# Performance work log

Measured on AMD Instinct MI355X. Metric: run time of the kernel, lower is better.

## Reference

```python
import jax, jax.numpy as jnp
from jax import lax
import numpy as np

K_IN, K_OUT, H, ML = 32, 16, 256, 80
L_PRE, L_FWD, B = 60, 80, 1024


def gru_cell(x, h, Wih, Whh, bih, bhh):
    # torch GRU gate order: r, z, n
    gi = x @ Wih.T + bih
    gh = h @ Whh.T + bhh
    ir, iz, inn = jnp.split(gi, 3, axis=-1)
    hr, hz, hn = jnp.split(gh, 3, axis=-1)
    r = jax.nn.sigmoid(ir + hr)
    z = jax.nn.sigmoid(iz + hz)
    n = jnp.tanh(inn + r * hn)
    return (1.0 - z) * n + z * h


def setup_inputs() -> dict:
    key = jax.random.key(0)
    ks = jax.random.split(key, 24)
    s = 0.05
    rn = lambda k, shp: (jax.random.normal(k, shp) * s).astype(jnp.float32)
    inp = {
        "pre_x": jax.random.normal(ks[0], (L_PRE, B, K_IN), dtype=jnp.float32),
        "pre_y": jax.random.normal(ks[1], (L_PRE, B, K_OUT), dtype=jnp.float32),
        "forward_x": jax.random.normal(ks[2], (L_FWD, B, K_IN), dtype=jnp.float32),
        # encoder: embedding Linear(k_in+k_out -> H), GRU(H,H)
        "enc_emb_W": rn(ks[3], (H, K_IN + K_OUT)),
        "enc_emb_b": rn(ks[4], (H,)),
        "enc_Wih": rn(ks[5], (3 * H, H)),
        "enc_Whh": rn(ks[6], (3 * H, H)),
        "enc_bih": rn(ks[7], (3 * H,)),
        "enc_bhh": rn(ks[8], (3 * H,)),
        # decoder: embedding Linear(k_out+k_in -> H), attn Linear(2H -> ML),
        # attn_combine Linear(2H -> H), GRU(H,H), out Linear(H -> k_out)
        "dec_emb_W": rn(ks[9], (H, K_OUT + K_IN)),
        "dec_emb_b": rn(ks[10], (H,)),
        "attn_W": rn(ks[11], (ML, 2 * H)),
        "attn_b": rn(ks[12], (ML,)),
        "comb_W": rn(ks[13], (H, 2 * H)),
        "comb_b": rn(ks[14], (H,)),
        "dec_Wih": rn(ks[15], (3 * H, H)),
        "dec_Whh": rn(ks[16], (3 * H, H)),
        "dec_bih": rn(ks[17], (3 * H,)),
        "dec_bhh": rn(ks[18], (3 * H,)),
        "out_W": rn(ks[19], (K_OUT, H)),
        "out_b": rn(ks[20], (K_OUT,)),
    }
    return inp


def reference(pre_x, pre_y, forward_x,
              enc_emb_W, enc_emb_b, enc_Wih, enc_Whh, enc_bih, enc_bhh,
              dec_emb_W, dec_emb_b, attn_W, attn_b, comb_W, comb_b,
              dec_Wih, dec_Whh, dec_bih, dec_bhh, out_W, out_b):
    L_pre, batch, _ = pre_x.shape
    hdim = enc_emb_b.shape[0]
    max_len = attn_b.shape[0]

    # ---- encoder ----
    emb = jnp.concatenate([pre_x, pre_y], axis=2) @ enc_emb_W.T + enc_emb_b  # [L_pre,B,H]
    h0 = jnp.zeros((batch, hdim), dtype=pre_x.dtype)

    def enc_step(h, x):
        h2 = gru_cell(x, h, enc_Wih, enc_Whh, enc_bih, enc_bhh)
        return h2, h2

    enc_h, enc_outs = lax.scan(enc_step, h0, emb)
    # pad encoder outputs to max_length along time (zeros beyond L_pre)
    enc_outputs = jnp.zeros((max_len, batch, hdim), dtype=pre_x.dtype).at[:L_pre].set(enc_outs)
    enc_bmh = enc_outputs.transpose(1, 0, 2)  # [B, ML, H]

    # ---- decoder (dropout inactive: eval mode) ----
    def dec_step(carry, fx):
        y, h = carry
        di = jnp.concatenate([y, fx], axis=-1)            # [B, k_out+k_in]
        e = di @ dec_emb_W.T + dec_emb_b                   # [B, H]
        logits = jnp.concatenate([e, h], axis=-1) @ attn_W.T + attn_b  # [B, ML]
        aw = jax.nn.softmax(logits, axis=-1)
        ctx = jnp.einsum('bm,bmh->bh', aw, enc_bmh)        # [B, H]
        g = jnp.tanh(jnp.concatenate([e, ctx], axis=-1) @ comb_W.T + comb_b)
        h2 = gru_cell(g, h, dec_Wih, dec_Whh, dec_bih, dec_bhh)
        y2 = h2 @ out_W.T + out_b                          # [B, k_out]
        return (y2, h2), y2

    y_init = jnp.zeros_like(pre_y[0])
    _, ys = lax.scan(dec_step, (y_init, enc_h), forward_x)
    return ys  # [L_fwd, B, k_out]
```

## Files before the change

kernel.cpp:

```cpp
#include <hip/hip_runtime.h>
#include <hip/hip_bf16.h>

#define BATCH 1024
#define HD 256
#define MLEN 80
#define LPRE 60
#define LFWD 80
#define KIN 32
#define KOUT 16

typedef unsigned short bf16_t;
typedef __attribute__((ext_vector_type(8))) short bf16x8;
typedef __attribute__((ext_vector_type(4))) float f32x4;
typedef __attribute__((ext_vector_type(4))) unsigned u32x4;

#define MFMA __builtin_amdgcn_mfma_f32_16x16x32_bf16

__device__ __forceinline__ float bf2f(bf16_t v){ return __uint_as_float(((unsigned)v)<<16); }
__device__ __forceinline__ bf16_t f2bf(float f){
    unsigned u = __float_as_uint(f);
    return (bf16_t)((u + 0x7FFFu + ((u>>16)&1u)) >> 16);
}
__device__ __forceinline__ unsigned pack2(float lo, float hi){
    return (unsigned)f2bf(lo) | ((unsigned)f2bf(hi)<<16);
}
__device__ __forceinline__ float bflo(unsigned d){ return __uint_as_float(d<<16); }
__device__ __forceinline__ float bfhi(unsigned d){ return __uint_as_float(d & 0xffff0000u); }
__device__ __forceinline__ float sigm(float x){ return 1.0f/(1.0f+__expf(-x)); }

#define OFF_Z  262144
#define OFF_IN 524288
#define OFF_HN 655360

__global__ void pack_gru(const float* __restrict__ Wih, const float* __restrict__ Whh,
                         bf16_t* __restrict__ dst)
{
    int T = blockIdx.x*256 + threadIdx.x;
    int grp, local;
    if (T < 16384){ grp=0; local=T; }
    else if (T < 32768){ grp=1; local=T-16384; }
    else if (T < 40960){ grp=2; local=T-32768; }
    else { grp=3; local=T-40960; }
    int nkt = (grp<2)?16:8;
    int nt  = local / (nkt*64);
    int rem = local - nt*(nkt*64);
    int kt  = rem >> 6;
    int l   = rem & 63;
    int n   = nt*16 + (l&15);
    int k0  = kt*32 + ((l>>4)<<3);
    unsigned w[4];
    #pragma unroll
    for (int h2=0; h2<4; h2++){
        float v[2];
        #pragma unroll
        for (int s=0; s<2; s++){
            int k = k0 + h2*2 + s;
            if (grp==0)      v[s] = (k<256)? Wih[(size_t)n*HD + k]       : Whh[(size_t)n*HD + (k-256)];
            else if (grp==1) v[s] = (k<256)? Wih[(size_t)(256+n)*HD + k] : Whh[(size_t)(256+n)*HD + (k-256)];
            else if (grp==2) v[s] = Wih[(size_t)(512+n)*HD + k];
            else             v[s] = Whh[(size_t)(512+n)*HD + k];
        }
        w[h2] = pack2(v[0], v[1]);
    }
    uint4 u = {w[0],w[1],w[2],w[3]};
    *(uint4*)((char*)dst + (size_t)T*16) = u;
}

__global__ void pack_B512(const float* __restrict__ W, bf16_t* __restrict__ dst)
{
    int T = blockIdx.x*256 + threadIdx.x;
    int nt = T >> 10, kt = (T>>6)&15, l = T&63;
    int n = nt*16 + (l&15);
    int k0 = kt*32 + ((l>>4)<<3);
    unsigned w[4];
    #pragma unroll
    for (int h2=0; h2<4; h2++)
        w[h2] = pack2(W[(size_t)n*512 + k0+h2*2], W[(size_t)n*512 + k0+h2*2+1]);
    uint4 u = {w[0],w[1],w[2],w[3]};
    *(uint4*)((char*)dst + (size_t)T*16) = u;
}

__global__ void wfuse_kernel(const float* __restrict__ dembW, const float* __restrict__ dembB,
                             const float* __restrict__ outW, const float* __restrict__ outB,
                             float* __restrict__ Wfuse, float* __restrict__ ebias)
{
    int T = blockIdx.x*256 + threadIdx.x;
    if (T < 65536){
        int k = T >> 8, n = T & 255;
        float acc = 0.f;
        #pragma unroll
        for (int o=0;o<16;o++) acc += dembW[(size_t)n*48 + o]*outW[(size_t)o*HD + k];
        Wfuse[(size_t)k*HD + n] = acc;
    } else if (T < 65792){
        int n = T - 65536;
        float acc = dembB[n];
        #pragma unroll
        for (int o=0;o<16;o++) acc += outB[o]*dembW[(size_t)n*48 + o];
        ebias[n] = acc;
    }
}

__global__ void pack_logits(const float* __restrict__ Wfuse, const float* __restrict__ dembW,
                            const float* __restrict__ attW, const float* __restrict__ attB,
                            const float* __restrict__ dembB, const float* __restrict__ ebias,
                            bf16_t* __restrict__ BL, bf16_t* __restrict__ BL0,
                            float* __restrict__ lb, float* __restrict__ lb0)
{
    int T = blockIdx.x*256 + threadIdx.x;
    if (T < 5760){
        int variant = (T < 2880) ? 0 : 1;
        int local = variant ? (T-2880) : T;
        int nt = local/576, rem = local - nt*576;
        int kt = rem >> 6, l = rem & 63;
        int m  = nt*16 + (l&15);
        int k0 = kt*32 + ((l>>4)<<3);
        unsigned w[4];
        #pragma unroll
        for (int h2=0; h2<4; h2++){
            float v[2];
            for (int s=0;s<2;s++){
                int k = k0 + h2*2 + s;
                float acc;
                if (kt < 8){
                    if (variant == 0){
                        acc = attW[(size_t)m*512 + 256 + k];
                        for (int n=0;n<256;n++) acc += Wfuse[(size_t)k*HD + n]*attW[(size_t)m*512 + n];
                    } else {
                        acc = attW[(size_t)m*512 + 256 + k];
                    }
                } else {
                    int kp = k - 256;
                    acc = 0.f;
                    for (int n=0;n<256;n++) acc += dembW[(size_t)n*48 + 16 + kp]*attW[(size_t)m*512 + n];
                }
                v[s] = acc;
            }
            w[h2] = pack2(v[0], v[1]);
        }
        uint4 u = {w[0],w[1],w[2],w[3]};
        bf16_t* d = variant ? BL0 : BL;
        *(uint4*)((char*)d + (size_t)local*16) = u;
    } else if (T < 5840){
        int m = T - 5760;
        float acc = attB[m];
        for (int n=0;n<256;n++) acc += ebias[n]*attW[(size_t)m*512 + n];
        lb[m] = acc;
    } else if (T < 5920){
        int m = T - 5840;
        float acc = attB[m];
        for (int n=0;n<256;n++) acc += dembB[n]*attW[(size_t)m*512 + n];
        lb0[m] = acc;
    }
}

__global__ void pack_gfold(const float* __restrict__ Wfuse, const float* __restrict__ dembW,
                           const float* __restrict__ combW, const float* __restrict__ combB,
                           const float* __restrict__ ebias, const float* __restrict__ dembB,
                           bf16_t* __restrict__ dst, float* __restrict__ cbf, float* __restrict__ cbf0)
{
    int T = blockIdx.x*256 + threadIdx.x;
    if (T < 9216){
        int nt = T/576, rem = T - nt*576;
        int kt = rem >> 6, l = rem & 63;
        int n = nt*16 + (l&15);
        int k0 = kt*32 + ((l>>4)<<3);
        unsigned w[4];
        for (int h2=0; h2<4; h2++){
            float v[2];
            for (int s=0;s<2;s++){
                int k = k0 + h2*2 + s;
                float acc = 0.f;
                if (k < 256){
                    for (int j=0;j<256;j++) acc += Wfuse[(size_t)k*HD + j]*combW[(size_t)n*512 + j];
                } else {
                    int kp = k - 256;
                    for (int j=0;j<256;j++) acc += dembW[(size_t)j*48 + 16 + kp]*combW[(size_t)n*512 + j];
                }
                v[s] = acc;
            }
            w[h2] = pack2(v[0], v[1]);
        }
        uint4 u = {w[0],w[1],w[2],w[3]};
        *(uint4*)((char*)dst + (size_t)T*16) = u;
    } else if (T < 9472){
        int n = T - 9216;
        float acc = combB[n];
        for (int j=0;j<256;j++) acc += ebias[j]*combW[(size_t)n*512 + j];
        cbf[n] = acc;
    } else if (T < 9728){
        int n = T - 9472;
        float acc = combB[n];
        for (int j=0;j<256;j++) acc += dembB[j]*combW[(size_t)n*512 + j];
        cbf0[n] = acc;
    }
}

__global__ void pack_out(const float* __restrict__ outW, bf16_t* __restrict__ dst)
{
    int T = blockIdx.x*256 + threadIdx.x;
    int kt = T >> 6, l = T & 63;
    int n  = l & 15;
    int k0 = kt*32 + ((l>>4)<<3);
    unsigned w[4];
    #pragma unroll
    for (int h2=0; h2<4; h2++)
        w[h2] = pack2(outW[(size_t)n*HD + k0+h2*2], outW[(size_t)n*HD + k0+h2*2+1]);
    uint4 u = {w[0],w[1],w[2],w[3]};
    *(uint4*)((char*)dst + (size_t)T*16) = u;
}

__global__ __launch_bounds__(256) void emb_kernel(
    const float* __restrict__ px, const float* __restrict__ py,
    const float* __restrict__ embW, const float* __restrict__ embB,
    bf16_t* __restrict__ emb)
{
    __shared__ float Ws[256*49];
    __shared__ float xy[16][48];
    __shared__ float bs[256];
    int t = blockIdx.y, b0 = blockIdx.x*16, tid = threadIdx.x;
    for (int i = tid; i < 256*48; i += 256){ int n=i/48, k=i-n*48; Ws[n*49+k]=embW[i]; }
    bs[tid] = embB[tid];
    for (int i = tid; i < 16*48; i += 256){
        int r=i/48, k=i-r*48;
        xy[r][k] = (k<KIN)? px[((size_t)t*BATCH + b0+r)*KIN + k]
                          : py[((size_t)t*BATCH + b0+r)*KOUT + (k-KIN)];
    }
    __syncthreads();
    int n = tid;
    const float* w = &Ws[n*49];
    for (int r=0;r<16;r++){
        float acc = bs[n];
        #pragma unroll
        for (int k=0;k<48;k++) acc += xy[r][k]*w[k];
        emb[((size_t)t*BATCH + b0+r)*HD + n] = f2bf(acc);
    }
}

__global__ void fxconv(const float* __restrict__ fx, bf16_t* __restrict__ dst)
{
    size_t i = (size_t)blockIdx.x*256 + threadIdx.x;
    const float4* s = (const float4*)(fx + i*8);
    float4 a = s[0], b = s[1];
    uint4 u = { pack2(a.x,a.y), pack2(a.z,a.w), pack2(b.x,b.y), pack2(b.z,b.w) };
    *(uint4*)(dst + i*8) = u;
}

__global__ __launch_bounds__(256) void pgemm(
    const bf16_t* __restrict__ enc, const bf16_t* __restrict__ Bcmb,
    bf16_t* __restrict__ P)
{
    __shared__ __align__(16) bf16_t As[16][264];
    __shared__ __align__(16) bf16_t Gs[16][264];
    int tid = threadIdx.x, b0 = blockIdx.x*16, t = blockIdx.y;
    const bf16_t* src = enc + ((size_t)t*BATCH + b0)*HD;
    for (int i = tid; i < 512; i += 256){
        int r = i>>5, c = i&31;
        *(uint4*)&As[r][c*8] = *(const uint4*)(src + (size_t)r*HD + c*8);
    }
    __syncthreads();
    int lane = tid&63, wave = tid>>6;
    const bf16_t* arow = &As[lane&15][(lane>>4)*8];
    size_t loff = (size_t)lane*16;
    #pragma unroll
    for (int u=0; u<4; u++){
        int nt = wave*4 + u;
        f32x4 c = {0,0,0,0};
        #pragma unroll
        for (int k8=0; k8<8; k8++){
            bf16x8 a = *(const bf16x8*)(arow + k8*32);
            bf16x8 b = *(const bf16x8*)((const char*)Bcmb + (size_t)(((nt<<4)+8+k8)<<10) + loff);
            c = MFMA(a, b, c, 0,0,0);
        }
        int n = (nt<<4) + (lane&15);
        #pragma unroll
        for (int q=0;q<4;q++) Gs[((lane>>4)<<2)+q][n] = f2bf(c[q]);
    }
    __syncthreads();
    bf16_t* dst = P + ((size_t)t*BATCH + b0)*HD;
    for (int i = tid; i < 512; i += 256){
        int r = i>>5, c = i&31;
        *(uint4*)(dst + (size_t)r*HD + c*8) = *(const uint4*)&Gs[r][c*8];
    }
}

__global__ __launch_bounds__(512) void gru_step2(
    const bf16_t* __restrict__ A0, const bf16_t* __restrict__ A1,
    const bf16_t* __restrict__ Bp,
    const float* __restrict__ bih, const float* __restrict__ bhh,
    const float* __restrict__ hprev, float* __restrict__ hnext,
    bf16_t* __restrict__ hnext_bf, bf16_t* __restrict__ extra_bf)
{
    __shared__ __align__(16) bf16_t As[16][520];
    __shared__ __align__(16) f32x4 redR[4][64];
    __shared__ __align__(16) f32x4 redZ[4][64];
    __shared__ __align__(16) f32x4 redI[4][64];
    int tid = threadIdx.x, b0 = blockIdx.x*16;
    for (int i = tid; i < 1024; i += 512){
        int r = i>>6, c = i&63;
        const bf16_t* src = (c<32)? (A0 + (size_t)(b0+r)*HD + c*8)
                                  : (A1 + (size_t)(b0+r)*HD + (c-32)*8);
        *(uint4*)&As[r][c*8] = *(const uint4*)src;
    }
    __syncthreads();
    int lane = tid & 63, wave = tid >> 6;
    int pairId = wave >> 1, half = wave & 1;
    int jt = blockIdx.y*4 + pairId;
    const char* arow = (const char*)&As[lane&15][(lane>>4)*8];
    const char* bpc = (const char*)Bp;
    size_t loff = (size_t)lane*16;
    size_t offX = half ? (size_t)OFF_HN : (size_t)OFF_IN;
    int kt0 = half*8;
    f32x4 cr={0,0,0,0}, cz={0,0,0,0}, cx={0,0,0,0};
    #pragma unroll
    for (int k8=0; k8<8; k8++){
        int kt = kt0 + k8;
        bf16x8 a  = *(const bf16x8*)(arow + kt*64);
        bf16x8 br = *(const bf16x8*)(bpc + (size_t)(((jt<<4)+kt)<<10) + loff);
        bf16x8 bz = *(const bf16x8*)(bpc + OFF_Z + (size_t)(((jt<<4)+kt)<<10) + loff);
        bf16x8 bx = *(const bf16x8*)(bpc + offX + (size_t)(((jt<<3)+k8)<<10) + loff);
        cr = MFMA(a, br, cr, 0,0,0);
        cz = MFMA(a, bz, cz, 0,0,0);
        cx = MFMA(a, bx, cx, 0,0,0);
    }
    if (half == 0){
        redR[pairId][lane] = cr;
        redZ[pairId][lane] = cz;
        redI[pairId][lane] = cx;
    }
    __syncthreads();
    if (half == 1){
        f32x4 crA = redR[pairId][lane];
        f32x4 czA = redZ[pairId][lane];
        f32x4 ci  = redI[pairId][lane];
        int j = (jt<<4) + (lane&15);
        float b_r = bih[j] + bhh[j];
        float b_z = bih[256+j] + bhh[256+j];
        float b_i = bih[512+j], b_h = bhh[512+j];
        #pragma unroll
        for (int q=0;q<4;q++){
            int b = b0 + ((lane>>4)<<2) + q;
            float rv = sigm(cr[q] + crA[q] + b_r);
            float zv = sigm(cz[q] + czA[q] + b_z);
            float nv = tanhf(ci[q] + b_i + rv*(cx[q] + b_h));
            float h2 = (1.0f - zv)*nv + zv*hprev[(size_t)b*HD + j];
            hnext[(size_t)b*HD + j] = h2;
            bf16_t hb = f2bf(h2);
            hnext_bf[(size_t)b*HD + j] = hb;
            extra_bf[(size_t)b*HD + j] = hb;
        }
    }
}

__global__ __launch_bounds__(1024) void dec_front(
    const bf16_t* __restrict__ hbf, const bf16_t* __restrict__ fxt,
    const bf16_t* __restrict__ P,
    const bf16_t* __restrict__ BL, const bf16_t* __restrict__ Bgf,
    const bf16_t* __restrict__ Bout,
    const float* __restrict__ lbp, const float* __restrict__ cbf,
    const float* __restrict__ outB,
    int t, bf16_t* __restrict__ g_out, float* __restrict__ out)
{
    __shared__ __align__(16) bf16_t As[16][296];
    __shared__ float awL[16][84];
    __shared__ float Cpart[16][256];
    __shared__ float CbF[16][260];

    int tid = threadIdx.x, b0 = blockIdx.x*16;

    if (tid < 576){
        int r = tid/36, c = tid - r*36;
        const bf16_t* src = (c<32)? (hbf + (size_t)(b0+r)*HD + c*8)
                                  : (fxt + (size_t)(b0+r)*KIN + (c-32)*8);
        *(uint4*)&As[r][c*8] = *(const uint4*)src;
    }

    int half = tid >> 9;
    int u    = tid & 511;
    int cr_  = u >> 5;
    int cc0  = (u & 31) * 8;
    const bf16_t* cbp = P + ((size_t)(half*30)*BATCH + (b0+cr_))*HD + cc0;
    u32x4 pf[10];
    #pragma unroll
    for (int i=0;i<10;i++) pf[i] = *(const u32x4*)(cbp + (size_t)i*BATCH*HD);

    __syncthreads();

    int lane = tid & 63, wave = tid >> 6;
    const bf16_t* arow = &As[lane&15][(lane>>4)*8];
    size_t loff = (size_t)lane*16;
    int kt0 = t ? 0 : 8;

    if (wave < 5){
        f32x4 c = {0,0,0,0};
        #pragma unroll
        for (int kt = 0; kt < 9; kt++){
            bf16x8 a = *(const bf16x8*)(arow + kt*32);
            bf16x8 b = *(const bf16x8*)((const char*)BL + (size_t)((wave*9+kt)<<10) + loff);
            c = MFMA(a, b, c, 0,0,0);
        }
        int m = (wave<<4) + (lane&15);
        float bbm = lbp[m];
        #pragma unroll
        for (int q=0;q<4;q++) awL[((lane>>4)<<2)+q][m] = c[q] + bbm;
    } else if (wave == 5 && t > 0){
        f32x4 c = {0,0,0,0};
        #pragma unroll
        for (int kt = 0; kt < 8; kt++){
            bf16x8 a = *(const bf16x8*)(arow + kt*32);
            bf16x8 b = *(const bf16x8*)((const char*)Bout + (size_t)(kt<<10) + loff);
            c = MFMA(a, b, c, 0,0,0);
        }
        int o = lane & 15;
        float bo = outB[o];
        #pragma unroll
        for (int q=0;q<4;q++){
            int r = ((lane>>4)<<2) + q;
            out[((size_t)(t-1)*BATCH + b0+r)*KOUT + o] = c[q] + bo;
        }
    }
    __syncthreads();

    if (tid < 256){
        int r2 = tid >> 4, l2 = tid & 15;
        float vmax = -1e30f;
        for (int m=l2; m<80; m+=16) vmax = fmaxf(vmax, awL[r2][m]);
        #pragma unroll
        for (int k=1; k<16; k<<=1) vmax = fmaxf(vmax, __shfl_xor(vmax, k, 16));
        float ps = 0.f;
        for (int m=l2; m<80; m+=16){ float v = __expf(awL[r2][m]-vmax); awL[r2][m]=v; ps += v; }
        #pragma unroll
        for (int k=1; k<16; k<<=1) ps += __shfl_xor(ps, k, 16);
        float inv = 1.0f/ps;
        for (int m=l2; m<80; m+=16) awL[r2][m] *= inv;
    }
    __syncthreads();

    float acc[8];
    #pragma unroll
    for (int i=0;i<8;i++) acc[i] = 0.f;
    {
        const float* awr = &awL[cr_][half*30];
        #pragma unroll
        for (int i=0;i<10;i++){
            float w = awr[i];
            acc[0]=fmaf(w,bflo(pf[i][0]),acc[0]); acc[1]=fmaf(w,bfhi(pf[i][0]),acc[1]);
            acc[2]=fmaf(w,bflo(pf[i][1]),acc[2]); acc[3]=fmaf(w,bfhi(pf[i][1]),acc[3]);
            acc[4]=fmaf(w,bflo(pf[i][2]),acc[4]); acc[5]=fmaf(w,bfhi(pf[i][2]),acc[5]);
            acc[6]=fmaf(w,bflo(pf[i][3]),acc[6]); acc[7]=fmaf(w,bfhi(pf[i][3]),acc[7]);
        }
        #pragma unroll 5
        for (int i=10;i<30;i++){
            u32x4 v = *(const u32x4*)(cbp + (size_t)i*BATCH*HD);
            float w = awr[i];
            acc[0]=fmaf(w,bflo(v[0]),acc[0]); acc[1]=fmaf(w,bfhi(v[0]),acc[1]);
            acc[2]=fmaf(w,bflo(v[1]),acc[2]); acc[3]=fmaf(w,bfhi(v[1]),acc[3]);
            acc[4]=fmaf(w,bflo(v[2]),acc[4]); acc[5]=fmaf(w,bfhi(v[2]),acc[5]);
            acc[6]=fmaf(w,bflo(v[3]),acc[6]); acc[7]=fmaf(w,bfhi(v[3]),acc[7]);
        }
    }
    if (half == 0){
        float4 p0 = {acc[0],acc[1],acc[2],acc[3]};
        float4 p1 = {acc[4],acc[5],acc[6],acc[7]};
        *(float4*)&Cpart[cr_][cc0]   = p0;
        *(float4*)&Cpart[cr_][cc0+4] = p1;
    }
    __syncthreads();

    if (half == 1){
        float4 p0 = *(const float4*)&Cpart[cr_][cc0];
        float4 p1 = *(const float4*)&Cpart[cr_][cc0+4];
        float4 o0 = {acc[0]+p0.x, acc[1]+p0.y, acc[2]+p0.z, acc[3]+p0.w};
        float4 o1 = {acc[4]+p1.x, acc[5]+p1.y, acc[6]+p1.z, acc[7]+p1.w};
        *(float4*)&CbF[cr_][cc0]   = o0;
        *(float4*)&CbF[cr_][cc0+4] = o1;
    }
    __syncthreads();

    {
        f32x4 c = {0,0,0,0};
        for (int kt=kt0; kt<9; kt++){
            bf16x8 a = *(const bf16x8*)(arow + kt*32);
            bf16x8 b = *(const bf16x8*)((const char*)Bgf + (size_t)((wave*9+kt)<<10) + loff);
            c = MFMA(a, b, c, 0,0,0);
        }
        int n = (wave<<4) + (lane&15);
        float bb = cbf[n];
        #pragma unroll
        for (int q=0;q<4;q++){
            int r = ((lane>>4)<<2) + q;
            g_out[(size_t)(b0+r)*HD + n] = f2bf(tanhf(c[q] + CbF[r][n] + bb));
        }
    }
}

__global__ __launch_bounds__(256) void final79(
    const float* __restrict__ hf, const float* __restrict__ outW,
    const float* __restrict__ outB, float* __restrict__ ys)
{
    __shared__ float hs[16][260];
    __shared__ float ow[16*260];
    int tid = threadIdx.x, b0 = blockIdx.x*16;
    for (int i=tid;i<4096;i+=256){ int o2=i>>8,k=i&255; ow[o2*260+k]=outW[(size_t)o2*HD+k]; }
    for (int i=tid;i<4096;i+=256){ int r=i>>8,k=i&255; hs[r][k]=hf[(size_t)(b0+r)*HD+k]; }
    __syncthreads();
    int r=tid>>4, o=tid&15;
    float acc=outB[o];
    const float* w=&ow[o*260];
    for(int k=0;k<256;k++) acc += hs[r][k]*w[k];
    ys[((size_t)79*BATCH + b0+r)*KOUT + o] = acc;
}

extern "C" void kernel_launch(void* const* d_in, const int* in_sizes, int n_in,
                              void* d_out, int out_size, void* d_ws, size_t ws_size,
                              hipStream_t stream) {
    const float* pre_x    = (const float*)d_in[0];
    const float* pre_y    = (const float*)d_in[1];
    const float* fwd_x    = (const float*)d_in[2];
    const float* enc_embW = (const float*)d_in[3];
    const float* enc_embB = (const float*)d_in[4];
    const float* enc_Wih  = (const float*)d_in[5];
    const float* enc_Whh  = (const float*)d_in[6];
    const float* enc_bih  = (const float*)d_in[7];
    const float* enc_bhh  = (const float*)d_in[8];
    const float* dec_embW = (const float*)d_in[9];
    const float* dec_embB = (const float*)d_in[10];
    const float* attn_W   = (const float*)d_in[11];
    const float* attn_b   = (const float*)d_in[12];
    const float* comb_W   = (const float*)d_in[13];
    const float* comb_b   = (const float*)d_in[14];
    const float* dec_Wih  = (const float*)d_in[15];
    const float* dec_Whh  = (const float*)d_in[16];
    const float* dec_bih  = (const float*)d_in[17];
    const float* dec_bhh  = (const float*)d_in[18];
    const float* out_W    = (const float*)d_in[19];
    const float* out_b    = (const float*)d_in[20];
    float* out = (float*)d_out;

    char* ws = (char*)d_ws;
    size_t o = 0;
    auto alloc = [&](size_t bytes)->char*{
        char* p = ws + o; o = (o + bytes + 255) & ~(size_t)255; return p;
    };
    bf16_t* EMB     = (bf16_t*)alloc((size_t)LPRE*BATCH*HD*2);
    bf16_t* ENC_OUT = (bf16_t*)alloc((size_t)LPRE*BATCH*HD*2);
    bf16_t* PBUF    = (bf16_t*)alloc((size_t)LPRE*BATCH*HD*2);
    bf16_t* FXB     = (bf16_t*)alloc((size_t)LFWD*BATCH*KIN*2);
    float*  HF0     = (float*) alloc((size_t)BATCH*HD*4);
    float*  HF1     = (float*) alloc((size_t)BATCH*HD*4);
    bf16_t* HB0     = (bf16_t*)alloc((size_t)BATCH*HD*2);
    bf16_t* HB1     = (bf16_t*)alloc((size_t)BATCH*HD*2);
    bf16_t* GBUF    = (bf16_t*)alloc((size_t)BATCH*HD*2);
    bf16_t* DUMMY   = (bf16_t*)alloc((size_t)BATCH*HD*2);
    float*  WFUSE   = (float*) alloc((size_t)256*256*4);
    float*  EBIAS   = (float*) alloc(256*4);
    float*  LB      = (float*) alloc(80*4);
    float*  LB0     = (float*) alloc(80*4);
    float*  CBF     = (float*) alloc(256*4);
    float*  CBF0    = (float*) alloc(256*4);
    bf16_t* PACK_ENC = (bf16_t*)alloc(786432);
    bf16_t* PACK_DEC = (bf16_t*)alloc(786432);
    bf16_t* PACK_CMB = (bf16_t*)alloc(262144);
    bf16_t* PACK_GF  = (bf16_t*)alloc(147456);
    bf16_t* PACK_BL  = (bf16_t*)alloc(46080);
    bf16_t* PACK_BL0 = (bf16_t*)alloc(46080);
    bf16_t* PACK_OUT = (bf16_t*)alloc(8192);

    hipMemsetAsync(HF0, 0, (size_t)BATCH*HD*4, stream);
    hipMemsetAsync(HB0, 0, (size_t)BATCH*HD*2, stream);

    dim3 blk(256);
    emb_kernel<<<dim3(64,60), blk, 0, stream>>>(pre_x, pre_y, enc_embW, enc_embB, EMB);
    fxconv<<<dim3(1280), blk, 0, stream>>>(fwd_x, FXB);
    pack_gru<<<dim3(192), blk, 0, stream>>>(enc_Wih, enc_Whh, PACK_ENC);
    pack_gru<<<dim3(192), blk, 0, stream>>>(dec_Wih, dec_Whh, PACK_DEC);
    pack_B512<<<dim3(64), blk, 0, stream>>>(comb_W, PACK_CMB);
    wfuse_kernel<<<dim3(257), blk, 0, stream>>>(dec_embW, dec_embB, out_W, out_b, WFUSE, EBIAS);
    pack_logits<<<dim3(24), blk, 0, stream>>>(WFUSE, dec_embW, attn_W, attn_b, dec_embB,
                                              EBIAS, PACK_BL, PACK_BL0, LB, LB0);
    pack_gfold<<<dim3(38), blk, 0, stream>>>(WFUSE, dec_embW, comb_W, comb_b,
                                             EBIAS, dec_embB, PACK_GF, CBF, CBF0);
    pack_out<<<dim3(2), blk, 0, stream>>>(out_W, PACK_OUT);

    float*  HF[2] = {HF0, HF1};
    bf16_t* HB[2] = {HB0, HB1};
    int p = 0;

    for (int t = 0; t < LPRE; t++){
        gru_step2<<<dim3(64,4), dim3(512), 0, stream>>>(
            EMB + (size_t)t*BATCH*HD, HB[p], PACK_ENC, enc_bih, enc_bhh,
            HF[p], HF[p^1], HB[p^1], ENC_OUT + (size_t)t*BATCH*HD);
        p ^= 1;
    }
    pgemm<<<dim3(64,60), blk, 0, stream>>>(ENC_OUT, PACK_CMB, PBUF);

    for (int t = 0; t < LFWD; t++){
        const bf16_t* fxt = FXB + (size_t)t*BATCH*KIN;
        dec_front<<<dim3(64), dim3(1024), 0, stream>>>(
            HB[p], fxt, PBUF,
            t ? PACK_BL : PACK_BL0, PACK_GF, PACK_OUT,
            t ? LB : LB0, t ? CBF : CBF0, out_b,
            t, GBUF, out);
        gru_step2<<<dim3(64,4), dim3(512), 0, stream>>>(
            GBUF, HB[p], PACK_DEC, dec_bih, dec_bhh,
            HF[p], HF[p^1], HB[p^1], DUMMY);
        p ^= 1;
    }
    final79<<<dim3(64), blk, 0, stream>>>(HF[p], out_W, out_b, out);
}
```

Baseline: 2.391 ms.

## Fuse decoder GRU cell into dec_front kernel, keeping g in shared memory

Merges the per-step decoder GRU update into the decoder front kernel. The combined activation g now stays in shared memory instead of going through a global buffer, and one of the two launches per decode step goes away. Each block of 16 waves now computes all 256 hidden columns for 16 batch rows, with every wave covering a 16-column slice of the r/z/n gates. The cost is parallelism: the separate GRU kernel ran on a 64x4 grid, while the fused one runs on only 64 blocks, so each block does more serial MFMA work and loads all of the GRU weights.

```diff
diff --git a/kernel.cpp b/kernel.cpp
--- a/kernel.cpp
+++ b/kernel.cpp
@@ -351,16 +351,20 @@
     }
 }
 
-__global__ __launch_bounds__(1024) void dec_front(
+__global__ __launch_bounds__(1024) void dec_step(
     const bf16_t* __restrict__ hbf, const bf16_t* __restrict__ fxt,
     const bf16_t* __restrict__ P,
     const bf16_t* __restrict__ BL, const bf16_t* __restrict__ Bgf,
-    const bf16_t* __restrict__ Bout,
+    const bf16_t* __restrict__ Bout, const bf16_t* __restrict__ Bgru,
     const float* __restrict__ lbp, const float* __restrict__ cbf,
+    const float* __restrict__ dbih, const float* __restrict__ dbhh,
     const float* __restrict__ outB,
-    int t, bf16_t* __restrict__ g_out, float* __restrict__ out)
+    const float* __restrict__ hprev, float* __restrict__ hnext,
+    bf16_t* __restrict__ hnext_bf,
+    int t, float* __restrict__ out)
 {
     __shared__ __align__(16) bf16_t As[16][296];
+    __shared__ __align__(16) bf16_t Gs[16][264];
     __shared__ float awL[16][84];
     __shared__ float Cpart[16][256];
     __shared__ float CbF[16][260];
@@ -488,7 +492,45 @@
         #pragma unroll
         for (int q=0;q<4;q++){
             int r = ((lane>>4)<<2) + q;
-            g_out[(size_t)(b0+r)*HD + n] = f2bf(tanhf(c[q] + CbF[r][n] + bb));
+            Gs[r][n] = f2bf(tanhf(c[q] + CbF[r][n] + bb));
+        }
+    }
+    __syncthreads();
+
+    {
+        const bf16_t* grow = &Gs[lane&15][(lane>>4)*8];
+        const char* bpc = (const char*)Bgru;
+        int jt = wave;
+        f32x4 cr={0,0,0,0}, cz={0,0,0,0}, ci={0,0,0,0}, ch={0,0,0,0};
+        #pragma unroll
+        for (int kt=0; kt<16; kt++){
+            bf16x8 a = (kt<8)? *(const bf16x8*)(grow + kt*32)
+                             : *(const bf16x8*)(arow + (kt-8)*32);
+            bf16x8 br = *(const bf16x8*)(bpc + (size_t)(((jt<<4)+kt)<<10) + loff);
+            bf16x8 bz = *(const bf16x8*)(bpc + OFF_Z + (size_t)(((jt<<4)+kt)<<10) + loff);
+            cr = MFMA(a, br, cr, 0,0,0);
+            cz = MFMA(a, bz, cz, 0,0,0);
+            if (kt < 8){
+                bf16x8 bi = *(const bf16x8*)(bpc + OFF_IN + (size_t)(((jt<<3)+kt)<<10) + loff);
+                ci = MFMA(a, bi, ci, 0,0,0);
+            } else {
+                bf16x8 bh = *(const bf16x8*)(bpc + OFF_HN + (size_t)(((jt<<3)+kt-8)<<10) + loff);
+                ch = MFMA(a, bh, ch, 0,0,0);
+            }
+        }
+        int j = (jt<<4) + (lane&15);
+        float b_r = dbih[j] + dbhh[j];
+        float b_z = dbih[256+j] + dbhh[256+j];
+        float b_i = dbih[512+j], b_h = dbhh[512+j];
+        #pragma unroll
+        for (int q=0;q<4;q++){
+            int b = b0 + ((lane>>4)<<2) + q;
+            float rv = sigm(cr[q] + b_r);
+            float zv = sigm(cz[q] + b_z);
+            float nv = tanhf(ci[q] + b_i + rv*(ch[q] + b_h));
+            float h2 = (1.0f - zv)*nv + zv*hprev[(size_t)b*HD + j];
+            hnext[(size_t)b*HD + j] = h2;
+            hnext_bf[(size_t)b*HD + j] = f2bf(h2);
         }
     }
 }
@@ -549,8 +591,6 @@
     float*  HF1     = (float*) alloc((size_t)BATCH*HD*4);
     bf16_t* HB0     = (bf16_t*)alloc((size_t)BATCH*HD*2);
     bf16_t* HB1     = (bf16_t*)alloc((size_t)BATCH*HD*2);
-    bf16_t* GBUF    = (bf16_t*)alloc((size_t)BATCH*HD*2);
-    bf16_t* DUMMY   = (bf16_t*)alloc((size_t)BATCH*HD*2);
     float*  WFUSE   = (float*) alloc((size_t)256*256*4);
     float*  EBIAS   = (float*) alloc(256*4);
     float*  LB      = (float*) alloc(80*4);
@@ -595,14 +635,13 @@
 
     for (int t = 0; t < LFWD; t++){
         const bf16_t* fxt = FXB + (size_t)t*BATCH*KIN;
-        dec_front<<<dim3(64), dim3(1024), 0, stream>>>(
+        dec_step<<<dim3(64), dim3(1024), 0, stream>>>(
             HB[p], fxt, PBUF,
-            t ? PACK_BL : PACK_BL0, PACK_GF, PACK_OUT,
-            t ? LB : LB0, t ? CBF : CBF0, out_b,
-            t, GBUF, out);
-        gru_step2<<<dim3(64,4), dim3(512), 0, stream>>>(
-            GBUF, HB[p], PACK_DEC, dec_bih, dec_bhh,
-            HF[p], HF[p^1], HB[p^1], DUMMY);
+            t ? PACK_BL : PACK_BL0, PACK_GF, PACK_OUT, PACK_DEC,
+            t ? LB : LB0, t ? CBF : CBF0,
+            dec_bih, dec_bhh, out_b,
+            HF[p], HF[p^1], HB[p^1],
+            t, out);
         p ^= 1;
     }
     final79<<<dim3(64), blk, 0, stream>>>(HF[p], out_W, out_b, out);
```

New measurement: 2.623 ms. 9.7% more time.
